# Kernel optimization log

Hardware: AMD Instinct MI355X
Metric: run time of the kernel (lower is better)

## Reference

```python
import jax, jax.numpy as jnp
import numpy as np
import math

INF = 1e10

def setup_inputs() -> dict:
    key = jax.random.key(0)
    ks = jax.random.split(key, 6)
    B, S, T, D = 8, 1024, 1024, 1024
    stdv = 1.0 / math.sqrt(D)
    return {
        "key": jax.random.normal(ks[0], (B, S, D), dtype=jnp.float32),
        "mask_src": jnp.ones((B, S), dtype=jnp.float32),
        "mask_trg": jnp.ones((B, T), dtype=jnp.float32),
        "Wq": jax.random.uniform(ks[1], (D, D), jnp.float32, -stdv, stdv),
        "bq": jnp.zeros((D,), jnp.float32),
        "Wk": jax.random.uniform(ks[2], (D, D), jnp.float32, -stdv, stdv),
        "bk": jnp.zeros((D,), jnp.float32),
        "wg": jax.random.uniform(ks[3], (D,), jnp.float32, -stdv, stdv),
        "bg": jnp.zeros((1,), jnp.float32),
    }


def reference(key, mask_src, mask_trg, Wq, bq, Wk, bk, wg, bg):
    B, S, D = key.shape
    T = mask_trg.shape[1]
    scale = jnp.asarray(math.sqrt(D), key.dtype)

    # --- linear (position-based Gaussian) attention ---
    src_lens = mask_src.sum(-1)                      # [B]
    trg_lens = mask_trg.sum(-1)                      # [B]
    steps = src_lens / trg_lens                      # [B]
    idx_t = steps[:, None] * jnp.arange(T, dtype=key.dtype)[None, :]   # [B,T]
    idx_s = jnp.arange(S, dtype=key.dtype)                              # [S]
    dist2 = (idx_s[None, None, :] - idx_t[:, :, None]) ** 2            # [B,T,S]
    l_logits = -dist2 / 0.3 - INF * (1.0 - mask_src[:, None, :])
    l_att = jax.nn.softmax(l_logits, axis=-1)                           # [B,T,S]

    # query from position attention
    query = jnp.einsum('bts,bsd->btd', l_att, key)                      # [B,T,D]

    # learned gate, broadcast [B,T,1] -> [B,T,S]
    gates = jax.nn.sigmoid(query @ wg + bg)[:, :, None]                 # [B,T,1]

    # QK dot-product attention
    q = query @ Wq.T + bq                                               # [B,T,D]
    k = key @ Wk.T + bk                                                 # [B,S,D]
    dots = jnp.einsum('btd,bsd->bts', q, k)
    dots = dots - (1.0 - mask_src[:, None, :]) * INF
    probs = jax.nn.softmax(dots / scale, axis=-1)                       # [B,T,S]

    # gated mixture of QK attention and position attention
    return (1.0 - gates) * probs + gates * l_att
```

## Files before the change

### kernel.cpp

```cpp
#include <hip/hip_runtime.h>
#include <hip/hip_bf16.h>
#include <stdint.h>

typedef unsigned short ushort_t;

#define BB 8
#define SS 1024
#define TT 1024
#define DD 1024
#define INF_ 1e10f

__device__ __forceinline__ float b2f(ushort_t u){
  union { unsigned u32; float f; } x; x.u32 = ((unsigned)u) << 16; return x.f;
}
__device__ __forceinline__ ushort_t f2b(float f){
  union { float f; unsigned u; } x; x.f = f;
  unsigned r = x.u + 0x7FFFu + ((x.u >> 16) & 1u);
  return (ushort_t)(r >> 16);
}

__global__ __launch_bounds__(256) void pre_kernel(
    const float* __restrict__ Wq, const float* __restrict__ Wk,
    ushort_t* __restrict__ WqT, ushort_t* __restrict__ WkT,
    const float* __restrict__ msrc, const float* __restrict__ mtrg,
    float* __restrict__ steps, float* __restrict__ v2)
{
  __shared__ float tile[32][33];
  __shared__ float sh[8];
  int blk = blockIdx.x, tid = threadIdx.x;
  if (blk < 2048){
    const float* src = (blk >= 1024) ? Wk : Wq;
    ushort_t* dst = (blk >= 1024) ? WkT : WqT;
    int q = blk & 1023;
    int tx = q & 31, ty = q >> 5;
    int c = tid & 31, r0 = tid >> 5;
    #pragma unroll
    for (int k = 0; k < 4; k++){
      int r = r0 + k*8;
      tile[r][c] = src[(size_t)(ty*32 + r)*DD + tx*32 + c];
    }
    __syncthreads();
    #pragma unroll
    for (int k = 0; k < 4; k++){
      int r = r0 + k*8;
      dst[(size_t)(tx*32 + r)*DD + ty*32 + c] = f2b(tile[c][r]);
    }
  } else {
    int b = blk - 2048;
    if (b < 4) v2[b*256 + tid] = 0.f;
    float a = 0.f, c = 0.f;
    for (int i = tid; i < SS; i += 256) a += msrc[b*SS + i];
    for (int i = tid; i < TT; i += 256) c += mtrg[b*TT + i];
    #pragma unroll
    for (int o = 32; o; o >>= 1){ a += __shfl_xor(a, o); c += __shfl_xor(c, o); }
    int wv = tid >> 6, ln = tid & 63;
    if (!ln){ sh[wv] = a; sh[4+wv] = c; }
    __syncthreads();
    if (!tid){
      float sa = sh[0]+sh[1]+sh[2]+sh[3];
      float sc = sh[4]+sh[5]+sh[6]+sh[7];
      steps[b] = sa / sc;
    }
  }
}

__global__ __launch_bounds__(256) void v2_kernel(
    const float* __restrict__ Wk, const float* __restrict__ bq,
    float* __restrict__ v2)
{
  int tid = threadIdx.x;
  int f = tid * 4;
  int r0 = blockIdx.x * 32;
  float a0=0.f, a1=0.f, a2=0.f, a3=0.f;
  for (int r = 0; r < 32; r++){
    float s = bq[r0 + r];
    float4 w = *(const float4*)(Wk + (size_t)(r0 + r)*DD + f);
    a0 += s*w.x; a1 += s*w.y; a2 += s*w.z; a3 += s*w.w;
  }
  atomicAdd(&v2[f+0], a0); atomicAdd(&v2[f+1], a1);
  atomicAdd(&v2[f+2], a2); atomicAdd(&v2[f+3], a3);
}

__global__ __launch_bounds__(256) void key_convert_kernel(
    const float* __restrict__ key, const float* __restrict__ wg,
    const float* __restrict__ v2f, ushort_t* __restrict__ keyb,
    float* __restrict__ kw, float* __restrict__ cv)
{
  __shared__ float sh[8];
  int row = blockIdx.x;
  int tid = threadIdx.x, d0 = tid*4;
  float4 v = *(const float4*)(key + (size_t)row*DD + d0);
  ushort4 o; o.x=f2b(v.x); o.y=f2b(v.y); o.z=f2b(v.z); o.w=f2b(v.w);
  *(ushort4*)(keyb + (size_t)row*DD + d0) = o;
  float4 w4 = *(const float4*)(wg + d0);
  float4 u4 = *(const float4*)(v2f + d0);
  float pk = v.x*w4.x + v.y*w4.y + v.z*w4.z + v.w*w4.w;
  float pc = v.x*u4.x + v.y*u4.y + v.z*u4.z + v.w*u4.w;
  #pragma unroll
  for (int off = 32; off; off >>= 1){ pk += __shfl_xor(pk, off); pc += __shfl_xor(pc, off); }
  int wvv = tid >> 6;
  if ((tid & 63) == 0){ sh[wvv] = pk; sh[4+wvv] = pc; }
  __syncthreads();
  if (!tid){
    kw[row] = sh[0]+sh[1]+sh[2]+sh[3];
    cv[row] = sh[4]+sh[5]+sh[6]+sh[7];
  }
}

typedef __bf16 bf16x8 __attribute__((ext_vector_type(8)));
typedef float f32x4 __attribute__((ext_vector_type(4)));

#define CP16(g, l) __builtin_amdgcn_global_load_lds( \
    (const __attribute__((address_space(1))) void*)(g), \
    (__attribute__((address_space(3))) void*)(l), 16, 0, 0)

__global__ __launch_bounds__(256, 2) void gemm_bt_kernel(
    const ushort_t* __restrict__ A, const ushort_t* __restrict__ Bm,
    const float* __restrict__ bias, void* __restrict__ Cv,
    int M, int N, int K, int lda, int ldb,
    long long sA, long long sB, long long sC, int hasBias, int outBF16,
    int gx, int gxy)
{
  __shared__ ushort_t lA[128*32];
  __shared__ ushort_t lB[128*32];

  const int bpx = gridDim.x >> 3;
  const int lin = blockIdx.x;
  const int glob = (lin & 7) * bpx + (lin >> 3);
  const int bz = glob / gxy;
  const int rem = glob - bz * gxy;
  const int by = rem / gx;
  const int bx = rem - by * gx;

  A  += (size_t)bz * sA;
  Bm += (size_t)bz * sB;

  const int tid = threadIdx.x;
  const int wv = tid >> 6, ln = tid & 63;
  const int r4 = ln >> 2, c8 = (ln & 3) * 8;

  const ushort_t* gA0 = A  + (size_t)(by*128 + wv*32 + r4) * lda + c8;
  const ushort_t* gA1 = gA0 + (size_t)16 * lda;
  const ushort_t* gB0 = Bm + (size_t)(bx*128 + wv*32 + r4) * ldb + c8;
  const ushort_t* gB1 = gB0 + (size_t)16 * ldb;
  ushort_t* lA0 = &lA[(wv*32     ) * 32];
  ushort_t* lA1 = &lA[(wv*32 + 16) * 32];
  ushort_t* lB0 = &lB[(wv*32     ) * 32];
  ushort_t* lB1 = &lB[(wv*32 + 16) * 32];

  const int lm = ln & 15, qd = ln >> 4;
  const int wm = (wv >> 1) * 64, wn = (wv & 1) * 64;

  f32x4 acc[4][4];
  #pragma unroll
  for (int i = 0; i < 4; i++)
    #pragma unroll
    for (int j = 0; j < 4; j++) acc[i][j] = (f32x4){0.f, 0.f, 0.f, 0.f};

  for (int k0 = 0; k0 < K; k0 += 32){
    CP16(gA0, lA0); CP16(gA1, lA1); CP16(gB0, lB0); CP16(gB1, lB1);
    gA0 += 32; gA1 += 32; gB0 += 32; gB1 += 32;
    __syncthreads();
    bf16x8 af[4], bf[4];
    #pragma unroll
    for (int i = 0; i < 4; i++) af[i] = *(const bf16x8*)&lA[(wm + i*16 + lm)*32 + qd*8];
    #pragma unroll
    for (int j = 0; j < 4; j++) bf[j] = *(const bf16x8*)&lB[(wn + j*16 + lm)*32 + qd*8];
    #pragma unroll
    for (int i = 0; i < 4; i++)
      #pragma unroll
      for (int j = 0; j < 4; j++)
        acc[i][j] = __builtin_amdgcn_mfma_f32_16x16x32_bf16(af[i], bf[j], acc[i][j], 0, 0, 0);
    __syncthreads();
  }

  const int row0 = by*128 + wm + qd*4;
  const int col0 = bx*128 + wn + lm;
  ushort_t* Cb = (ushort_t*)Cv + (size_t)bz * sC;
  float*    Cf = (float*)Cv    + (size_t)bz * sC;
  #pragma unroll
  for (int j = 0; j < 4; j++){
    int col = col0 + j*16;
    float bv = hasBias ? bias[col] : 0.f;
    #pragma unroll
    for (int i = 0; i < 4; i++)
      #pragma unroll
      for (int r = 0; r < 4; r++){
        size_t idx = (size_t)(row0 + i*16 + r) * N + col;
        float v = acc[i][j][r] + bv;
        if (outBF16) Cb[idx] = f2b(v); else Cf[idx] = v;
      }
  }
}

#define G2_STAGE_A(sel, k0) do{ \
    ushort_t* _d = &lA3[(sel)*(256*64) + (w*8)*64]; \
    CP16(gA0 + (k0), _d); \
    CP16(gA1 + (k0), _d + 64*64); \
    CP16(gA2 + (k0), _d + 128*64); \
    CP16(gA3 + (k0), _d + 192*64); }while(0)
#define G2_STAGE_B(sel, k0) do{ \
    ushort_t* _d = &lB2[(sel)*(128*64) + (w*8)*64]; \
    CP16(gB0 + (k0), _d); \
    CP16(gB1 + (k0), _d + 64*64); }while(0)

__global__ __launch_bounds__(512, 2) void gemm256_kernel(
    const ushort_t* __restrict__ A, const ushort_t* __restrict__ Bm,
    ushort_t* __restrict__ C,
    int M, int N, int K, int lda, int ldb,
    long long sA, long long sB, long long sC, int gx, int gxy)
{
  __shared__ ushort_t lA3[3 * 256 * 64];
  __shared__ ushort_t lB2[2 * 128 * 64];
  (void)M;

  const int bpx = gridDim.x >> 3;
  const int lin = blockIdx.x;
  const int glob = (lin & 7) * bpx + (lin >> 3);
  const int bz = glob / gxy;
  const int rem = glob - bz * gxy;
  const int by = rem / gx;
  const int bx = rem - by * gx;

  A  += (size_t)bz * sA;
  Bm += (size_t)bz * sB;

  const int tid = threadIdx.x;
  const int w = tid >> 6, l = tid & 63;
  const int lm = l & 15, qd = l >> 4;
  const int wm = w >> 2, wn = w & 3;

  const int srow = l >> 3;
  const int sch  = (l & 7) ^ srow;

  const ushort_t* gA0 = A + (size_t)(by*256 +       w*8 + srow) * lda + sch*8;
  const ushort_t* gA1 = gA0 + (size_t)64  * lda;
  const ushort_t* gA2 = gA0 + (size_t)128 * lda;
  const ushort_t* gA3 = gA0 + (size_t)192 * lda;
  const ushort_t* gB0 = Bm + (size_t)(bx*128 +      w*8 + srow) * ldb + sch*8;
  const ushort_t* gB1 = gB0 + (size_t)64  * ldb;

  f32x4 acc[8][2];
  #pragma unroll
  for (int i = 0; i < 8; i++){ acc[i][0] = (f32x4){0.f,0.f,0.f,0.f}; acc[i][1] = (f32x4){0.f,0.f,0.f,0.f}; }

  G2_STAGE_A(0, 0);
  G2_STAGE_B(0, 0);
  G2_STAGE_A(1, 64);

  const int NT = K >> 6;
  int rdA = 0, stA = 2, rdB = 0;
  for (int t = 0; t < NT; ++t){
    if (t < NT - 1) asm volatile("s_waitcnt vmcnt(4)" ::: "memory");
    else            asm volatile("s_waitcnt vmcnt(0)" ::: "memory");
    __builtin_amdgcn_s_barrier();
    if (t + 1 < NT) G2_STAGE_B(rdB ^ 1, (t+1)*64);
    if (t + 2 < NT) G2_STAGE_A(stA,     (t+2)*64);

    const ushort_t* sa = &lA3[rdA*(256*64) + (wm*128)*64];
    const ushort_t* sb = &lB2[rdB*(128*64) + (wn*32)*64];
    #pragma unroll
    for (int ks = 0; ks < 2; ++ks){
      const int ch = ((ks << 2) | qd) ^ (lm & 7);
      bf16x8 af[8], bfr[2];
      #pragma unroll
      for (int i = 0; i < 8; i++) af[i]  = *(const bf16x8*)&sa[(i*16 + lm)*64 + ch*8];
      #pragma unroll
      for (int j = 0; j < 2; j++) bfr[j] = *(const bf16x8*)&sb[(j*16 + lm)*64 + ch*8];
      __builtin_amdgcn_s_setprio(1);
      #pragma unroll
      for (int i = 0; i < 8; i++)
        #pragma unroll
        for (int j = 0; j < 2; j++)
          acc[i][j] = __builtin_amdgcn_mfma_f32_16x16x32_bf16(af[i], bfr[j], acc[i][j], 0, 0, 0);
      __builtin_amdgcn_s_setprio(0);
    }
    rdA = (rdA == 2) ? 0 : rdA + 1;
    stA = (stA == 2) ? 0 : stA + 1;
    rdB ^= 1;
  }

  const int row0 = by*256 + wm*128 + qd*4;
  const int col0 = bx*128 + wn*32 + lm;
  ushort_t* Cp = C + (size_t)bz * sC;
  #pragma unroll
  for (int j = 0; j < 2; j++)
    #pragma unroll
    for (int i = 0; i < 8; i++)
      #pragma unroll
      for (int r = 0; r < 4; r++)
        Cp[(size_t)(row0 + i*16 + r) * N + col0 + j*16] = f2b(acc[i][j][r]);
}

__global__ __launch_bounds__(256) void wmt_reduce_kernel(
    const float* __restrict__ part, ushort_t* __restrict__ dst)
{
  int i4 = blockIdx.x * 256 + threadIdx.x;
  const float4* p = (const float4*)part;
  float4 a = p[i4];
  float4 b = p[i4 + 262144];
  float4 c = p[i4 + 524288];
  float4 d = p[i4 + 786432];
  ushort4 o;
  o.x = f2b(a.x + b.x + c.x + d.x);
  o.y = f2b(a.y + b.y + c.y + d.y);
  o.z = f2b(a.z + b.z + c.z + d.z);
  o.w = f2b(a.w + b.w + c.w + d.w);
  ((ushort4*)dst)[i4] = o;
}

__global__ __launch_bounds__(256) void band_kernel(
    const ushort_t* __restrict__ kmb, const float* __restrict__ mask_src,
    const float* __restrict__ steps, const float* __restrict__ kw,
    const float* __restrict__ bg, ushort_t* __restrict__ qm2b,
    float* __restrict__ gates)
{
  __shared__ float shw[8][17];
  __shared__ int shslo[8];
  int bx = blockIdx.x;
  int b = bx >> 7, t0 = (bx & 127) * 8;
  int tid = threadIdx.x;

  if (tid < 8){
    int t = t0 + tid;
    float c = steps[b] * (float)t;
    int slo = (int)ceilf(c - 8.0f);
    float w[17], m = -3e38f;
    #pragma unroll
    for (int i = 0; i < 17; i++){
      int s = slo + i;
      float l = -3e38f;
      if (s >= 0 && s < SS){
        float dd = (float)s - c;
        l = -dd*dd*(1.0f/0.3f) - INF_*(1.0f - mask_src[b*SS + s]);
      }
      w[i] = l; m = fmaxf(m, l);
    }
    float norm = 0.f, ga = 0.f;
    #pragma unroll
    for (int i = 0; i < 17; i++){
      float e = __expf(w[i] - m);
      int s = slo + i;
      if (s >= 0 && s < SS) ga += e * kw[b*SS + s]; else e = 0.f;
      w[i] = e; norm += e;
    }
    float inv = 1.0f / norm;
    #pragma unroll
    for (int i = 0; i < 17; i++) shw[tid][i] = w[i] * inv;
    shslo[tid] = slo;
    gates[b*TT + t] = 1.0f / (1.0f + __expf(-(ga*inv + bg[0])));
  }
  __syncthreads();

  int smin = shslo[0], smax = shslo[7] + 16;
  if (smin < 0) smin = 0;
  if (smax > SS-1) smax = SS-1;
  int d0 = tid * 4;
  float acc[8][4];
  #pragma unroll
  for (int t = 0; t < 8; t++){ acc[t][0]=0.f; acc[t][1]=0.f; acc[t][2]=0.f; acc[t][3]=0.f; }

  const ushort_t* kbase = kmb + ((size_t)b*SS)*DD + d0;
  for (int s = smin; s <= smax; s++){
    ushort4 kv = *(const ushort4*)(kbase + (size_t)s*DD);
    float k0 = b2f(kv.x), k1 = b2f(kv.y), k2 = b2f(kv.z), k3 = b2f(kv.w);
    #pragma unroll
    for (int t = 0; t < 8; t++){
      unsigned u = (unsigned)(s - shslo[t]);
      if (u < 17u){
        float wgt = shw[t][u];
        acc[t][0] += wgt*k0; acc[t][1] += wgt*k1; acc[t][2] += wgt*k2; acc[t][3] += wgt*k3;
      }
    }
  }
  #pragma unroll
  for (int t = 0; t < 8; t++){
    ushort4 o; o.x=f2b(acc[t][0]); o.y=f2b(acc[t][1]); o.z=f2b(acc[t][2]); o.w=f2b(acc[t][3]);
    *(ushort4*)(qm2b + ((size_t)(b*TT + t0 + t))*DD + d0) = o;
  }
}

__device__ __forceinline__ float blkmax(float v, float* sh){
  #pragma unroll
  for (int o = 32; o; o >>= 1) v = fmaxf(v, __shfl_xor(v, o));
  __syncthreads();
  if ((threadIdx.x & 63) == 0) sh[threadIdx.x >> 6] = v;
  __syncthreads();
  return fmaxf(fmaxf(sh[0], sh[1]), fmaxf(sh[2], sh[3]));
}
__device__ __forceinline__ float blksum(float v, float* sh){
  #pragma unroll
  for (int o = 32; o; o >>= 1) v += __shfl_xor(v, o);
  __syncthreads();
  if ((threadIdx.x & 63) == 0) sh[threadIdx.x >> 6] = v;
  __syncthreads();
  return sh[0] + sh[1] + sh[2] + sh[3];
}

__global__ __launch_bounds__(256) void softmax_mix_kernel(
    const ushort_t* __restrict__ dotsb, float* __restrict__ out,
    const float* __restrict__ mask_src, const float* __restrict__ steps,
    const float* __restrict__ gates, const float* __restrict__ cv)
{
  __shared__ float sh[4];
  int blk = blockIdx.x;
  int b = blk >> 10, t = blk & 1023;
  int tid = threadIdx.x;
  int s0 = tid * 4;
  float c = steps[b] * (float)t;

  ushort4 dv = *(const ushort4*)(dotsb + (size_t)blk*SS + s0);
  float4 mv = *(const float4*)(mask_src + (size_t)b*SS + s0);
  float4 cva = *(const float4*)(cv + (size_t)b*SS + s0);
  float dvf[4] = {b2f(dv.x) + cva.x, b2f(dv.y) + cva.y, b2f(dv.z) + cva.z, b2f(dv.w) + cva.w};
  float msk[4] = {mv.x, mv.y, mv.z, mv.w};
  float dl[4], ll[4];
  float dmax = -3e38f, lmax = -3e38f;
  #pragma unroll
  for (int r = 0; r < 4; r++){
    float im = INF_ * (1.0f - msk[r]);
    dl[r] = (dvf[r] - im) * (1.0f/32.0f);
    float dd = (float)(s0 + r) - c;
    ll[r] = -dd*dd*(1.0f/0.3f) - im;
    dmax = fmaxf(dmax, dl[r]);
    lmax = fmaxf(lmax, ll[r]);
  }
  float dm = blkmax(dmax, sh);
  float ps[4], lp[4];
  float psum = 0.f, lsum = 0.f;
  #pragma unroll
  for (int r = 0; r < 4; r++){ ps[r] = __expf(dl[r] - dm); psum += ps[r]; }
  psum = blksum(psum, sh);
  float lm2 = blkmax(lmax, sh);
  #pragma unroll
  for (int r = 0; r < 4; r++){ lp[r] = __expf(ll[r] - lm2); lsum += lp[r]; }
  lsum = blksum(lsum, sh);

  float g = gates[blk];
  float ip = (1.0f - g) / psum, il = g / lsum;
  float4 ov;
  ov.x = ps[0]*ip + lp[0]*il;
  ov.y = ps[1]*ip + lp[1]*il;
  ov.z = ps[2]*ip + lp[2]*il;
  ov.w = ps[3]*ip + lp[3]*il;
  *(float4*)(out + (size_t)blk*SS + s0) = ov;
}

extern "C" void kernel_launch(void* const* d_in, const int* in_sizes, int n_in,
                              void* d_out, int out_size, void* d_ws, size_t ws_size,
                              hipStream_t stream)
{
  const float* key      = (const float*)d_in[0];
  const float* mask_src = (const float*)d_in[1];
  const float* mask_trg = (const float*)d_in[2];
  const float* Wq       = (const float*)d_in[3];
  const float* bq       = (const float*)d_in[4];
  const float* Wk       = (const float*)d_in[5];
  const float* bk       = (const float*)d_in[6];
  const float* wg       = (const float*)d_in[7];
  const float* bg       = (const float*)d_in[8];
  float* out = (float*)d_out;
  (void)bk;

  char* ws = (char*)d_ws;
  float* steps     = (float*)ws;
  float* gates     = (float*)(ws + 4096);
  float* cv        = (float*)(ws + 4096 + 32768);
  float* kw        = (float*)(ws + 4096 + 65536);
  float* v2        = (float*)(ws + 4096 + 98304);
  ushort_t* WqTb   = (ushort_t*)(ws + 131072);
  ushort_t* WkTb   = WqTb + (size_t)DD*DD;
  ushort_t* WmTb   = WkTb + (size_t)DD*DD;
  ushort_t* keyb   = WmTb + (size_t)DD*DD;
  ushort_t* kmb    = keyb + (size_t)BB*SS*DD;
  char* shared16   = (char*)(kmb + (size_t)BB*SS*DD);
  float* wmPart    = (float*)shared16;
  ushort_t* qm2b   = (ushort_t*)shared16;
  ushort_t* dotsb  = kmb;

  pre_kernel<<<2056, 256, 0, stream>>>(Wq, Wk, WqTb, WkTb, mask_src, mask_trg, steps, v2);
  v2_kernel<<<32, 256, 0, stream>>>(Wk, bq, v2);
  key_convert_kernel<<<BB*SS, 256, 0, stream>>>(key, wg, v2, keyb, kw, cv);
  gemm_bt_kernel<<<256, 256, 0, stream>>>(
      WkTb, WqTb, nullptr, (void*)wmPart, DD, DD, DD/4, DD, DD,
      DD/4, DD/4, (long long)DD*DD, 0, 0, 8, 64);
  wmt_reduce_kernel<<<DD*DD/4/256, 256, 0, stream>>>(wmPart, WmTb);
  gemm256_kernel<<<256, 512, 0, stream>>>(
      keyb, WmTb, kmb, BB*SS, DD, DD, DD, DD, 0, 0, 0, 8, 256);
  band_kernel<<<BB*TT/8, 256, 0, stream>>>(kmb, mask_src, steps, kw, bg, qm2b, gates);
  gemm256_kernel<<<256, 512, 0, stream>>>(
      qm2b, keyb, dotsb, TT, SS, DD, DD, DD,
      (long long)TT*DD, (long long)SS*DD, (long long)TT*SS, 8, 32);
  softmax_mix_kernel<<<BB*TT, 256, 0, stream>>>(dotsb, out, mask_src, steps, gates, cv);
}
```

Before: 221.8 us.

## Triple-buffer B tile and interleave global prefetch with MFMA half-steps

Measured after the change: 211.8 us. -4.5%, faster.

```diff
diff --git a/kernel.cpp b/kernel.cpp
--- a/kernel.cpp
+++ b/kernel.cpp
@@ -193,16 +193,20 @@
   }
 }
 
-#define G2_STAGE_A(sel, k0) do{ \
+#define G2_STAGE_A(sel) do{ \
     ushort_t* _d = &lA3[(sel)*(256*64) + (w*8)*64]; \
-    CP16(gA0 + (k0), _d); \
-    CP16(gA1 + (k0), _d + 64*64); \
-    CP16(gA2 + (k0), _d + 128*64); \
-    CP16(gA3 + (k0), _d + 192*64); }while(0)
-#define G2_STAGE_B(sel, k0) do{ \
-    ushort_t* _d = &lB2[(sel)*(128*64) + (w*8)*64]; \
-    CP16(gB0 + (k0), _d); \
-    CP16(gB1 + (k0), _d + 64*64); }while(0)
+    CP16(gA0, _d); \
+    CP16(gA1, _d + 64*64); \
+    CP16(gA2, _d + 128*64); \
+    CP16(gA3, _d + 192*64); }while(0)
+#define G2_STAGE_B(sel) do{ \
+    ushort_t* _d = &lB3[(sel)*(128*64) + (w*8)*64]; \
+    CP16(gB0, _d); \
+    CP16(gB1, _d + 64*64); }while(0)
+#define G2_ADV() do{ gA0+=64; gA1+=64; gA2+=64; gA3+=64; gB0+=64; gB1+=64; }while(0)
+#define BAR()    asm volatile("s_barrier" ::: "memory")
+#define LGKM0()  do{ asm volatile("s_waitcnt lgkmcnt(0)" ::: "memory"); \
+                     __builtin_amdgcn_sched_barrier(0); }while(0)
 
 __global__ __launch_bounds__(512, 2) void gemm256_kernel(
     const ushort_t* __restrict__ A, const ushort_t* __restrict__ Bm,
@@ -211,7 +215,7 @@
     long long sA, long long sB, long long sC, int gx, int gxy)
 {
   __shared__ ushort_t lA3[3 * 256 * 64];
-  __shared__ ushort_t lB2[2 * 128 * 64];
+  __shared__ ushort_t lB3[3 * 128 * 64];
   (void)M;
 
   const int bpx = gridDim.x >> 3;
@@ -244,29 +248,29 @@
   #pragma unroll
   for (int i = 0; i < 8; i++){ acc[i][0] = (f32x4){0.f,0.f,0.f,0.f}; acc[i][1] = (f32x4){0.f,0.f,0.f,0.f}; }
 
-  G2_STAGE_A(0, 0);
-  G2_STAGE_B(0, 0);
-  G2_STAGE_A(1, 64);
+  G2_STAGE_A(0); G2_STAGE_B(0); G2_ADV();
+  G2_STAGE_A(1); G2_STAGE_B(1); G2_ADV();
+  asm volatile("s_waitcnt vmcnt(6)" ::: "memory");
+  BAR();
 
   const int NT = K >> 6;
-  int rdA = 0, stA = 2, rdB = 0;
+  int rd = 0, st = 2;
+  #pragma unroll 1
   for (int t = 0; t < NT; ++t){
-    if (t < NT - 1) asm volatile("s_waitcnt vmcnt(4)" ::: "memory");
-    else            asm volatile("s_waitcnt vmcnt(0)" ::: "memory");
-    __builtin_amdgcn_s_barrier();
-    if (t + 1 < NT) G2_STAGE_B(rdB ^ 1, (t+1)*64);
-    if (t + 2 < NT) G2_STAGE_A(stA,     (t+2)*64);
-
-    const ushort_t* sa = &lA3[rdA*(256*64) + (wm*128)*64];
-    const ushort_t* sb = &lB2[rdB*(128*64) + (wn*32)*64];
-    #pragma unroll
-    for (int ks = 0; ks < 2; ++ks){
-      const int ch = ((ks << 2) | qd) ^ (lm & 7);
+    const ushort_t* sa = &lA3[rd*(256*64) + (wm*128)*64];
+    const ushort_t* sb = &lB3[rd*(128*64) + (wn*32)*64];
+    const bool pre = (t + 2 < NT);
+
+    {
+      const int ch = qd ^ (lm & 7);
       bf16x8 af[8], bfr[2];
       #pragma unroll
       for (int i = 0; i < 8; i++) af[i]  = *(const bf16x8*)&sa[(i*16 + lm)*64 + ch*8];
       #pragma unroll
       for (int j = 0; j < 2; j++) bfr[j] = *(const bf16x8*)&sb[(j*16 + lm)*64 + ch*8];
+      if (pre) G2_STAGE_A(st);
+      BAR();
+      LGKM0();
       __builtin_amdgcn_s_setprio(1);
       #pragma unroll
       for (int i = 0; i < 8; i++)
@@ -274,10 +278,34 @@
         for (int j = 0; j < 2; j++)
           acc[i][j] = __builtin_amdgcn_mfma_f32_16x16x32_bf16(af[i], bfr[j], acc[i][j], 0, 0, 0);
       __builtin_amdgcn_s_setprio(0);
-    }
-    rdA = (rdA == 2) ? 0 : rdA + 1;
-    stA = (stA == 2) ? 0 : stA + 1;
-    rdB ^= 1;
+      BAR();
+    }
+    {
+      const int ch = (4 | qd) ^ (lm & 7);
+      bf16x8 af[8], bfr[2];
+      #pragma unroll
+      for (int i = 0; i < 8; i++) af[i]  = *(const bf16x8*)&sa[(i*16 + lm)*64 + ch*8];
+      #pragma unroll
+      for (int j = 0; j < 2; j++) bfr[j] = *(const bf16x8*)&sb[(j*16 + lm)*64 + ch*8];
+      if (pre) G2_STAGE_B(st);
+      BAR();
+      LGKM0();
+      __builtin_amdgcn_s_setprio(1);
+      #pragma unroll
+      for (int i = 0; i < 8; i++)
+        #pragma unroll
+        for (int j = 0; j < 2; j++)
+          acc[i][j] = __builtin_amdgcn_mfma_f32_16x16x32_bf16(af[i], bfr[j], acc[i][j], 0, 0, 0);
+      __builtin_amdgcn_s_setprio(0);
+    }
+    if (pre) G2_ADV();
+    if (t < NT - 1){
+      if (pre) asm volatile("s_waitcnt vmcnt(6)" ::: "memory");
+      else     asm volatile("s_waitcnt vmcnt(0)" ::: "memory");
+      BAR();
+    }
+    rd = (rd == 2) ? 0 : rd + 1;
+    st = (st == 2) ? 0 : st + 1;
   }
 
   const int row0 = by*256 + wm*128 + qd*4;
```
